# Kernel tuning notes

Measured on AMD Instinct MI355X. Metric: run time of the kernel, lower is better.

## Reference

```python
import jax, jax.numpy as jnp
import numpy as np

D_HEAD = 64
D_MODEL = 1024
N_HEADS = D_MODEL // D_HEAD
MAX_TOKENS = 2048


def setup_inputs() -> dict:
    key = jax.random.key(0)
    ks = jax.random.split(key, 5)
    batch, pos = 2, 2048
    # kaiming_normal_ on (n_heads, d_model, d_head): fan_in = d_model*d_head -> std = sqrt(2/fan_in)
    std_qkv = np.sqrt(2.0 / (D_MODEL * D_HEAD)).astype(np.float32)
    # xavier_normal_ on (d_model, d_model): std = sqrt(2/(fan_in+fan_out))
    std_out = np.sqrt(2.0 / (D_MODEL + D_MODEL)).astype(np.float32)
    return {
        "residual_stream": jax.random.normal(ks[0], (batch, pos, D_MODEL), dtype=jnp.float32),
        "weight_query": jax.random.normal(ks[1], (N_HEADS, D_MODEL, D_HEAD), dtype=jnp.float32) * std_qkv,
        "weight_key": jax.random.normal(ks[2], (N_HEADS, D_MODEL, D_HEAD), dtype=jnp.float32) * std_qkv,
        "weight_value": jax.random.normal(ks[3], (N_HEADS, D_MODEL, D_HEAD), dtype=jnp.float32) * std_qkv,
        "weight_out": jax.random.normal(ks[4], (D_MODEL, D_MODEL), dtype=jnp.float32) * std_out,
    }


def reference(residual_stream, weight_query, weight_key, weight_value, weight_out):
    # QKV projections: [b, p, m] x [h, m, d] -> [b, h, p, d]
    q = jnp.einsum('bpm,hmd->bhpd', residual_stream, weight_query)
    k = jnp.einsum('bpm,hmd->bhpd', residual_stream, weight_key)
    v = jnp.einsum('bpm,hmd->bhpd', residual_stream, weight_value)

    n_tokens = residual_stream.shape[1]
    # scaled scores [b, h, dest, src]
    scores = jnp.einsum('bhqd,bhkd->bhqk', q, k) / jnp.sqrt(jnp.float32(D_HEAD))
    # causal mask: -inf above the diagonal
    causal = jnp.tril(jnp.ones((n_tokens, n_tokens), dtype=bool))
    scores = jnp.where(causal, scores, jnp.float32(-jnp.inf))
    pattern = jax.nn.softmax(scores, axis=-1)

    attn = jnp.einsum('bhqk,bhkd->bhqd', pattern, v)  # [b, h, dest, d_head]
    # concat heads -> [b, p, h*d_head]
    b, h, p, d = attn.shape
    attn_concat = jnp.transpose(attn, (0, 2, 1, 3)).reshape(b, p, h * d)
    return jnp.einsum('bpm,mn->bpn', attn_concat, weight_out)
```

## Files before the change

kernel.cpp:

```cpp
#include <hip/hip_runtime.h>
#include <hip/hip_bf16.h>
#include <stdint.h>


typedef __bf16 bf16x8 __attribute__((ext_vector_type(8)));
typedef float f32x4 __attribute__((ext_vector_type(4)));
typedef unsigned short u16;

__device__ __forceinline__ u16 f2bf(float f) {
  unsigned u = __float_as_uint(f);
  u += 0x7fffu + ((u >> 16) & 1u);
  return (u16)(u >> 16);
}

__global__ __launch_bounds__(256) void xcvt_k(const float* __restrict__ in,
                                              u16* __restrict__ out) {
  int i = (blockIdx.x * 256 + threadIdx.x) * 8;
  float4 f0 = *reinterpret_cast<const float4*>(in + i);
  float4 f1 = *reinterpret_cast<const float4*>(in + i + 4);
  u16 tmp[8] = {f2bf(f0.x), f2bf(f0.y), f2bf(f0.z), f2bf(f0.w),
                f2bf(f1.x), f2bf(f1.y), f2bf(f1.z), f2bf(f1.w)};
  *reinterpret_cast<uint4*>(out + i) = *reinterpret_cast<uint4*>(tmp);
}

__global__ __launch_bounds__(256) void transpose_cvt_k(const float* __restrict__ in,
                                                       u16* __restrict__ out,
                                                       int R, int C) {
  __shared__ u16 tile[64][80];
  int b = blockIdx.z;
  int r0 = blockIdx.x * 64, c0 = blockIdx.y * 64;
  const float* ip = in + (size_t)b * R * C;
  u16* op = out + (size_t)b * R * C;
  int t = threadIdx.x;
  int r = t >> 2, cb = (t & 3) * 16;
  const float4* src = reinterpret_cast<const float4*>(ip + (size_t)(r0 + r) * C + c0 + cb);
  u16 tmp[16];
#pragma unroll
  for (int v = 0; v < 4; v++) {
    float4 f = src[v];
    tmp[v * 4 + 0] = f2bf(f.x);
    tmp[v * 4 + 1] = f2bf(f.y);
    tmp[v * 4 + 2] = f2bf(f.z);
    tmp[v * 4 + 3] = f2bf(f.w);
  }
  *reinterpret_cast<uint4*>(&tile[r][cb]) = *reinterpret_cast<uint4*>(&tmp[0]);
  *reinterpret_cast<uint4*>(&tile[r][cb + 8]) = *reinterpret_cast<uint4*>(&tmp[8]);
  __syncthreads();
  int c = t >> 2, rb = (t & 3) * 16;
  uint4 outv[2];
  u16* tp = reinterpret_cast<u16*>(outv);
#pragma unroll
  for (int j = 0; j < 16; j++) tp[j] = tile[rb + j][c];
  uint4* dst = reinterpret_cast<uint4*>(op + (size_t)(c0 + c) * R + r0 + rb);
  dst[0] = outv[0];
  dst[1] = outv[1];
}

__global__ __launch_bounds__(256) void transpose_qkv_k(const float* __restrict__ Wq,
                                                       const float* __restrict__ Wk,
                                                       const float* __restrict__ Wv,
                                                       u16* __restrict__ outBase) {
  __shared__ u16 tile[64][80];
  int z = blockIdx.z;
  int sel = z >> 4, head = z & 15;
  const float* W = (sel == 0) ? Wq : (sel == 1 ? Wk : Wv);
  const float* ip = W + (size_t)head * 65536;
  u16* op = outBase + (size_t)sel * 1048576 + (size_t)head * 65536;
  int r0 = blockIdx.x * 64;
  int t = threadIdx.x;
  int r = t >> 2, cb = (t & 3) * 16;
  const float4* src = reinterpret_cast<const float4*>(ip + (size_t)(r0 + r) * 64 + cb);
  u16 tmp[16];
#pragma unroll
  for (int v = 0; v < 4; v++) {
    float4 f = src[v];
    tmp[v * 4 + 0] = f2bf(f.x);
    tmp[v * 4 + 1] = f2bf(f.y);
    tmp[v * 4 + 2] = f2bf(f.z);
    tmp[v * 4 + 3] = f2bf(f.w);
  }
  *reinterpret_cast<uint4*>(&tile[r][cb]) = *reinterpret_cast<uint4*>(&tmp[0]);
  *reinterpret_cast<uint4*>(&tile[r][cb + 8]) = *reinterpret_cast<uint4*>(&tmp[8]);
  __syncthreads();
  int c = t >> 2, rb = (t & 3) * 16;
  uint4 outv[2];
  u16* tp = reinterpret_cast<u16*>(outv);
#pragma unroll
  for (int j = 0; j < 16; j++) tp[j] = tile[rb + j][c];
  uint4* dst = reinterpret_cast<uint4*>(op + (size_t)c * 1024 + r0 + rb);
  dst[0] = outv[0];
  dst[1] = outv[1];
}

__device__ __forceinline__ void gemm128_core(const u16* __restrict__ A,
                                             const u16* __restrict__ BT,
                                             int m0, int n0,
                                             f32x4 (&acc)[4][4]) {
  __shared__ u16 As[128][72];
  __shared__ u16 Bs[128][72];
  int t = threadIdx.x, l = t & 63;
  int w = t >> 6, wm = w & 1, wn = w >> 1;
  int l15 = l & 15, q4 = l >> 4;
  int sr = t >> 1, sch = (t & 1) * 32;
  f32x4 z4 = {0.f, 0.f, 0.f, 0.f};
#pragma unroll
  for (int mi = 0; mi < 4; mi++)
#pragma unroll
    for (int nt = 0; nt < 4; nt++) acc[mi][nt] = z4;

  for (int k0 = 0; k0 < 1024; k0 += 64) {
    __syncthreads();
    {
      const uint4* sa = reinterpret_cast<const uint4*>(A + (size_t)(m0 + sr) * 1024 + k0 + sch);
      const uint4* sb = reinterpret_cast<const uint4*>(BT + (size_t)(n0 + sr) * 1024 + k0 + sch);
      uint4 a0 = sa[0], a1 = sa[1], a2 = sa[2], a3 = sa[3];
      uint4 b0 = sb[0], b1 = sb[1], b2 = sb[2], b3 = sb[3];
      uint4* da = reinterpret_cast<uint4*>(&As[sr][sch]);
      da[0] = a0; da[1] = a1; da[2] = a2; da[3] = a3;
      uint4* db = reinterpret_cast<uint4*>(&Bs[sr][sch]);
      db[0] = b0; db[1] = b1; db[2] = b2; db[3] = b3;
    }
    __syncthreads();
#pragma unroll
    for (int kk = 0; kk < 2; kk++) {
      bf16x8 af[4], bfr[4];
#pragma unroll
      for (int mi = 0; mi < 4; mi++)
        af[mi] = *reinterpret_cast<const bf16x8*>(&As[wm * 64 + mi * 16 + l15][kk * 32 + q4 * 8]);
#pragma unroll
      for (int nt = 0; nt < 4; nt++)
        bfr[nt] = *reinterpret_cast<const bf16x8*>(&Bs[wn * 64 + nt * 16 + l15][kk * 32 + q4 * 8]);
#pragma unroll
      for (int mi = 0; mi < 4; mi++)
#pragma unroll
        for (int nt = 0; nt < 4; nt++)
          acc[mi][nt] = __builtin_amdgcn_mfma_f32_16x16x32_bf16(af[mi], bfr[nt], acc[mi][nt], 0, 0, 0);
    }
  }
}

__global__ __launch_bounds__(256) void qkv_gemm128_k(const u16* __restrict__ A,
                                                     const u16* __restrict__ BT,
                                                     u16* __restrict__ Q,
                                                     u16* __restrict__ K,
                                                     u16* __restrict__ VT2) {
  const float QSCALE = 0.125f * 1.44269504088896340736f;
  int m0 = blockIdx.x * 128, n0 = blockIdx.y * 128;
  f32x4 acc[4][4];
  gemm128_core(A, BT, m0, n0, acc);
  int t = threadIdx.x, l = t & 63;
  int w = t >> 6, wm = w & 1, wn = w >> 1;
  int l15 = l & 15, q4 = l >> 4;
#pragma unroll
  for (int mi = 0; mi < 4; mi++) {
#pragma unroll
    for (int nt = 0; nt < 4; nt++) {
#pragma unroll
      for (int r = 0; r < 4; r++) {
        int m = m0 + wm * 64 + mi * 16 + q4 * 4 + r;
        int n = n0 + wn * 64 + nt * 16 + l15;
        int wsel = n >> 10, h = (n >> 6) & 15, d = n & 63;
        int b = m >> 11, p = m & 2047;
        size_t bh = (size_t)(b * 16 + h);
        float v = acc[mi][nt][r];
        if (wsel == 0)
          Q[(bh * 2048 + p) * 64 + d] = f2bf(v * QSCALE);
        else if (wsel == 1)
          K[(bh * 2048 + p) * 64 + d] = f2bf(v);
        else
          VT2[((bh * 32 + (p >> 6)) * 64 + d) * 64 + (p & 63)] = f2bf(v);
      }
    }
  }
}

__global__ __launch_bounds__(256) void out_gemm128_k(const u16* __restrict__ A,
                                                     const u16* __restrict__ BT,
                                                     float* __restrict__ O) {
  int m0 = blockIdx.x * 128, n0 = blockIdx.y * 128;
  f32x4 acc[4][4];
  gemm128_core(A, BT, m0, n0, acc);
  int t = threadIdx.x, l = t & 63;
  int w = t >> 6, wm = w & 1, wn = w >> 1;
  int l15 = l & 15, q4 = l >> 4;
#pragma unroll
  for (int mi = 0; mi < 4; mi++) {
#pragma unroll
    for (int nt = 0; nt < 4; nt++) {
#pragma unroll
      for (int r = 0; r < 4; r++) {
        int m = m0 + wm * 64 + mi * 16 + q4 * 4 + r;
        int n = n0 + wn * 64 + nt * 16 + l15;
        O[(size_t)m * 1024 + n] = acc[mi][nt][r];
      }
    }
  }
}

__global__ __launch_bounds__(256) void attn_k(const u16* __restrict__ Q,
                                              const u16* __restrict__ K,
                                              const u16* __restrict__ VT2,
                                              u16* __restrict__ A) {
  __shared__ u16 Ks[2][64][72];
  __shared__ u16 Vs[2][64][72];
  __shared__ u16 P[4][16][72];
  int pr = blockIdx.x, h = blockIdx.y, b = blockIdx.z;
  size_t bh = (size_t)(b * 16 + h);
  const u16* Qp = Q + bh * 2048 * 64;
  const u16* Kp = K + bh * 2048 * 64;
  const u16* Vt = VT2 + bh * 32 * 64 * 64;
  int t = threadIdx.x, l = t & 63, w = t >> 6;
  int l15 = l & 15, q4 = l >> 4;
  const float NEG = -1e30f;
  f32x4 z4 = {0.f, 0.f, 0.f, 0.f};
  int srow = (t & 127) >> 1, shalf = t & 1;
  bool isV = t >= 128;
  const u16* sbase = (isV ? Vt : Kp) + (size_t)srow * 64 + shalf * 32;

#pragma unroll
  for (int which = 0; which < 2; which++) {
    int qt = which ? (31 - pr) : pr;
    int qrow = qt * 64 + w * 16 + l15;
    bf16x8 qf0 = *reinterpret_cast<const bf16x8*>(Qp + (size_t)qrow * 64 + q4 * 8);
    bf16x8 qf1 = *reinterpret_cast<const bf16x8*>(Qp + (size_t)qrow * 64 + 32 + q4 * 8);

    f32x4 accO[4] = {z4, z4, z4, z4};
    float rs[4] = {0.f, 0.f, 0.f, 0.f};

    {
      const uint4* s4 = reinterpret_cast<const uint4*>(sbase);
      uint4 v0 = s4[0], v1 = s4[1], v2 = s4[2], v3 = s4[3];
      uint4* d4 = isV ? reinterpret_cast<uint4*>(&Vs[0][srow][shalf * 32])
                      : reinterpret_cast<uint4*>(&Ks[0][srow][shalf * 32]);
      d4[0] = v0; d4[1] = v1; d4[2] = v2; d4[3] = v3;
    }
    __syncthreads();

    for (int kt = 0; kt <= qt; kt++) {
      int cur = kt & 1;
      bool more = kt < qt;
      uint4 n0, n1, n2, n3;
      if (more) {
        const uint4* s4 = reinterpret_cast<const uint4*>(sbase + (size_t)(kt + 1) * 4096);
        n0 = s4[0]; n1 = s4[1]; n2 = s4[2]; n3 = s4[3];
      }

      f32x4 s[4] = {z4, z4, z4, z4};
      __builtin_amdgcn_s_setprio(1);
#pragma unroll
      for (int kk = 0; kk < 2; kk++) {
        bf16x8 qa = (kk == 0) ? qf0 : qf1;
#pragma unroll
        for (int nt = 0; nt < 4; nt++) {
          bf16x8 kf = *reinterpret_cast<const bf16x8*>(&Ks[cur][nt * 16 + l15][kk * 32 + q4 * 8]);
          s[nt] = __builtin_amdgcn_mfma_f32_16x16x32_bf16(qa, kf, s[nt], 0, 0, 0);
        }
      }
      __builtin_amdgcn_s_setprio(0);
      if (kt == qt) {
        int rowl = w * 16 + q4 * 4;
#pragma unroll
        for (int nt = 0; nt < 4; nt++)
#pragma unroll
          for (int r = 0; r < 4; r++)
            if (nt * 16 + l15 > rowl + r) s[nt][r] = NEG;
      }
#pragma unroll
      for (int nt = 0; nt < 4; nt++)
#pragma unroll
        for (int r = 0; r < 4; r++) {
          float p = exp2f(s[nt][r]);
          rs[r] += p;
          P[w][q4 * 4 + r][nt * 16 + l15] = f2bf(p);
        }
      __builtin_amdgcn_s_setprio(1);
#pragma unroll
      for (int kk = 0; kk < 2; kk++) {
        bf16x8 pa = *reinterpret_cast<const bf16x8*>(&P[w][l15][kk * 32 + q4 * 8]);
#pragma unroll
        for (int nt = 0; nt < 4; nt++) {
          bf16x8 vf = *reinterpret_cast<const bf16x8*>(&Vs[cur][nt * 16 + l15][kk * 32 + q4 * 8]);
          accO[nt] = __builtin_amdgcn_mfma_f32_16x16x32_bf16(pa, vf, accO[nt], 0, 0, 0);
        }
      }
      __builtin_amdgcn_s_setprio(0);

      if (more) {
        uint4* d4 = isV ? reinterpret_cast<uint4*>(&Vs[cur ^ 1][srow][shalf * 32])
                        : reinterpret_cast<uint4*>(&Ks[cur ^ 1][srow][shalf * 32]);
        d4[0] = n0; d4[1] = n1; d4[2] = n2; d4[3] = n3;
      }
      __syncthreads();
    }
#pragma unroll
    for (int r = 0; r < 4; r++) {
#pragma unroll
      for (int sh = 1; sh < 16; sh <<= 1) rs[r] += __shfl_xor(rs[r], sh, 64);
      float inv = 1.f / rs[r];
      int prow = qt * 64 + w * 16 + q4 * 4 + r;
      size_t base = ((size_t)(b * 2048 + prow)) * 1024 + h * 64;
#pragma unroll
      for (int nt = 0; nt < 4; nt++) A[base + nt * 16 + l15] = f2bf(accO[nt][r] * inv);
    }
  }
}

extern "C" void kernel_launch(void* const* d_in, const int* in_sizes, int n_in,
                              void* d_out, int out_size, void* d_ws, size_t ws_size,
                              hipStream_t stream) {
  const float* X  = (const float*)d_in[0];
  const float* Wq = (const float*)d_in[1];
  const float* Wk = (const float*)d_in[2];
  const float* Wv = (const float*)d_in[3];
  const float* Wo = (const float*)d_in[4];
  float* out = (float*)d_out;

  u16* ws = (u16*)d_ws;
  u16* WqT = ws;
  u16* WoT = WqT + 3145728;
  u16* Xb  = WoT + 1048576;
  u16* Qb  = Xb + 4194304;
  u16* Kb  = Qb + 4194304;
  u16* VT2 = Kb + 4194304;
  u16* Ab  = Xb;

  xcvt_k<<<dim3(2048), 256, 0, stream>>>(X, Xb);
  transpose_qkv_k<<<dim3(16, 1, 48), 256, 0, stream>>>(Wq, Wk, Wv, WqT);
  transpose_cvt_k<<<dim3(16, 16, 1), 256, 0, stream>>>(Wo, WoT, 1024, 1024);

  qkv_gemm128_k<<<dim3(32, 24), 256, 0, stream>>>(Xb, WqT, Qb, Kb, VT2);
  attn_k<<<dim3(16, 16, 2), 256, 0, stream>>>(Qb, Kb, VT2, Ab);
  out_gemm128_k<<<dim3(32, 8), 256, 0, stream>>>(Ab, WoT, out);
}
```

Before: 205.3 us.

## Enlarge attention query tile to 128 rows and use direct global-to-LDS loads in GEMM

The attention kernel now handles 128 query rows per block, 32 per wave as two MFMA row groups. Each K/V tile in LDS is therefore reused across twice as many queries, and the grid is halved. Separately, the GEMM core stages A and B tiles with global_load_lds builtins into unpadded LDS arrays instead of loading through registers. The trade-offs are fewer blocks for occupancy and load balance in attention, more registers per wave, and possible LDS bank conflicts from the unpadded 64-wide rows.

```diff
diff --git a/kernel.cpp b/kernel.cpp
--- a/kernel.cpp
+++ b/kernel.cpp
@@ -92,16 +92,25 @@
   dst[1] = outv[1];
 }
 
+__device__ __forceinline__ void gload16(const u16* g, u16* l) {
+  __builtin_amdgcn_global_load_lds(
+      (__attribute__((address_space(1))) void*)(g),
+      (__attribute__((address_space(3))) void*)(l), 16, 0, 0);
+}
+
 __device__ __forceinline__ void gemm128_core(const u16* __restrict__ A,
                                              const u16* __restrict__ BT,
                                              int m0, int n0,
                                              f32x4 (&acc)[4][4]) {
-  __shared__ u16 As[128][72];
-  __shared__ u16 Bs[128][72];
+  __shared__ __align__(16) u16 As[128][64];
+  __shared__ __align__(16) u16 Bs[128][64];
   int t = threadIdx.x, l = t & 63;
   int w = t >> 6, wm = w & 1, wn = w >> 1;
   int l15 = l & 15, q4 = l >> 4;
-  int sr = t >> 1, sch = (t & 1) * 32;
+  int srow = w * 32 + (l >> 3);
+  int scol = (l & 7) * 8;
+  const u16* ga = A + (size_t)(m0 + srow) * 1024 + scol;
+  const u16* gb = BT + (size_t)(n0 + srow) * 1024 + scol;
   f32x4 z4 = {0.f, 0.f, 0.f, 0.f};
 #pragma unroll
   for (int mi = 0; mi < 4; mi++)
@@ -110,15 +119,10 @@
 
   for (int k0 = 0; k0 < 1024; k0 += 64) {
     __syncthreads();
-    {
-      const uint4* sa = reinterpret_cast<const uint4*>(A + (size_t)(m0 + sr) * 1024 + k0 + sch);
-      const uint4* sb = reinterpret_cast<const uint4*>(BT + (size_t)(n0 + sr) * 1024 + k0 + sch);
-      uint4 a0 = sa[0], a1 = sa[1], a2 = sa[2], a3 = sa[3];
-      uint4 b0 = sb[0], b1 = sb[1], b2 = sb[2], b3 = sb[3];
-      uint4* da = reinterpret_cast<uint4*>(&As[sr][sch]);
-      da[0] = a0; da[1] = a1; da[2] = a2; da[3] = a3;
-      uint4* db = reinterpret_cast<uint4*>(&Bs[sr][sch]);
-      db[0] = b0; db[1] = b1; db[2] = b2; db[3] = b3;
+#pragma unroll
+    for (int i = 0; i < 4; i++) {
+      gload16(ga + (size_t)(i * 8) * 1024 + k0, &As[w * 32 + i * 8][0]);
+      gload16(gb + (size_t)(i * 8) * 1024 + k0, &Bs[w * 32 + i * 8][0]);
     }
     __syncthreads();
 #pragma unroll
@@ -203,7 +207,7 @@
                                               u16* __restrict__ A) {
   __shared__ u16 Ks[2][64][72];
   __shared__ u16 Vs[2][64][72];
-  __shared__ u16 P[4][16][72];
+  __shared__ u16 P[4][32][80];
   int pr = blockIdx.x, h = blockIdx.y, b = blockIdx.z;
   size_t bh = (size_t)(b * 16 + h);
   const u16* Qp = Q + bh * 2048 * 64;
@@ -219,13 +223,25 @@
 
 #pragma unroll
   for (int which = 0; which < 2; which++) {
-    int qt = which ? (31 - pr) : pr;
-    int qrow = qt * 64 + w * 16 + l15;
-    bf16x8 qf0 = *reinterpret_cast<const bf16x8*>(Qp + (size_t)qrow * 64 + q4 * 8);
-    bf16x8 qf1 = *reinterpret_cast<const bf16x8*>(Qp + (size_t)qrow * 64 + 32 + q4 * 8);
-
-    f32x4 accO[4] = {z4, z4, z4, z4};
-    float rs[4] = {0.f, 0.f, 0.f, 0.f};
+    int qt = which ? (15 - pr) : pr;
+    int nkt = 2 * qt + 2;
+    int qr0 = qt * 128 + w * 32;
+    bf16x8 qf[2][2];
+#pragma unroll
+    for (int mi = 0; mi < 2; mi++) {
+      const u16* qp = Qp + (size_t)(qr0 + mi * 16 + l15) * 64;
+      qf[mi][0] = *reinterpret_cast<const bf16x8*>(qp + q4 * 8);
+      qf[mi][1] = *reinterpret_cast<const bf16x8*>(qp + 32 + q4 * 8);
+    }
+    f32x4 accO[2][4];
+    float rs[2][4];
+#pragma unroll
+    for (int mi = 0; mi < 2; mi++) {
+#pragma unroll
+      for (int nt = 0; nt < 4; nt++) accO[mi][nt] = z4;
+#pragma unroll
+      for (int r = 0; r < 4; r++) rs[mi][r] = 0.f;
+    }
 
     {
       const uint4* s4 = reinterpret_cast<const uint4*>(sbase);
@@ -236,51 +252,68 @@
     }
     __syncthreads();
 
-    for (int kt = 0; kt <= qt; kt++) {
+    for (int kt = 0; kt < nkt; kt++) {
       int cur = kt & 1;
-      bool more = kt < qt;
+      bool more = kt < nkt - 1;
       uint4 n0, n1, n2, n3;
       if (more) {
         const uint4* s4 = reinterpret_cast<const uint4*>(sbase + (size_t)(kt + 1) * 4096);
         n0 = s4[0]; n1 = s4[1]; n2 = s4[2]; n3 = s4[3];
       }
 
-      f32x4 s[4] = {z4, z4, z4, z4};
+      f32x4 s[2][4];
+#pragma unroll
+      for (int mi = 0; mi < 2; mi++)
+#pragma unroll
+        for (int nt = 0; nt < 4; nt++) s[mi][nt] = z4;
       __builtin_amdgcn_s_setprio(1);
 #pragma unroll
       for (int kk = 0; kk < 2; kk++) {
-        bf16x8 qa = (kk == 0) ? qf0 : qf1;
-#pragma unroll
-        for (int nt = 0; nt < 4; nt++) {
-          bf16x8 kf = *reinterpret_cast<const bf16x8*>(&Ks[cur][nt * 16 + l15][kk * 32 + q4 * 8]);
-          s[nt] = __builtin_amdgcn_mfma_f32_16x16x32_bf16(qa, kf, s[nt], 0, 0, 0);
-        }
+        bf16x8 kf[4];
+#pragma unroll
+        for (int nt = 0; nt < 4; nt++)
+          kf[nt] = *reinterpret_cast<const bf16x8*>(&Ks[cur][nt * 16 + l15][kk * 32 + q4 * 8]);
+#pragma unroll
+        for (int mi = 0; mi < 2; mi++)
+#pragma unroll
+          for (int nt = 0; nt < 4; nt++)
+            s[mi][nt] = __builtin_amdgcn_mfma_f32_16x16x32_bf16(qf[mi][kk], kf[nt], s[mi][nt], 0, 0, 0);
       }
       __builtin_amdgcn_s_setprio(0);
-      if (kt == qt) {
-        int rowl = w * 16 + q4 * 4;
+      if (kt >= 2 * qt) {
+        int colbase = (kt - 2 * qt) * 64;
+        int rowl = w * 32 + q4 * 4;
+#pragma unroll
+        for (int mi = 0; mi < 2; mi++)
+#pragma unroll
+          for (int nt = 0; nt < 4; nt++)
+#pragma unroll
+            for (int r = 0; r < 4; r++)
+              if (colbase + nt * 16 + l15 > rowl + mi * 16 + r) s[mi][nt][r] = NEG;
+      }
+#pragma unroll
+      for (int mi = 0; mi < 2; mi++)
 #pragma unroll
         for (int nt = 0; nt < 4; nt++)
 #pragma unroll
-          for (int r = 0; r < 4; r++)
-            if (nt * 16 + l15 > rowl + r) s[nt][r] = NEG;
-      }
-#pragma unroll
-      for (int nt = 0; nt < 4; nt++)
-#pragma unroll
-        for (int r = 0; r < 4; r++) {
-          float p = exp2f(s[nt][r]);
-          rs[r] += p;
-          P[w][q4 * 4 + r][nt * 16 + l15] = f2bf(p);
-        }
+          for (int r = 0; r < 4; r++) {
+            float p = exp2f(s[mi][nt][r]);
+            rs[mi][r] += p;
+            P[w][mi * 16 + q4 * 4 + r][nt * 16 + l15] = f2bf(p);
+          }
       __builtin_amdgcn_s_setprio(1);
 #pragma unroll
       for (int kk = 0; kk < 2; kk++) {
-        bf16x8 pa = *reinterpret_cast<const bf16x8*>(&P[w][l15][kk * 32 + q4 * 8]);
+        bf16x8 pa[2];
+#pragma unroll
+        for (int mi = 0; mi < 2; mi++)
+          pa[mi] = *reinterpret_cast<const bf16x8*>(&P[w][mi * 16 + l15][kk * 32 + q4 * 8]);
 #pragma unroll
         for (int nt = 0; nt < 4; nt++) {
           bf16x8 vf = *reinterpret_cast<const bf16x8*>(&Vs[cur][nt * 16 + l15][kk * 32 + q4 * 8]);
-          accO[nt] = __builtin_amdgcn_mfma_f32_16x16x32_bf16(pa, vf, accO[nt], 0, 0, 0);
+#pragma unroll
+          for (int mi = 0; mi < 2; mi++)
+            accO[mi][nt] = __builtin_amdgcn_mfma_f32_16x16x32_bf16(pa[mi], vf, accO[mi][nt], 0, 0, 0);
         }
       }
       __builtin_amdgcn_s_setprio(0);
@@ -293,15 +326,18 @@
       __syncthreads();
     }
 #pragma unroll
-    for (int r = 0; r < 4; r++) {
-#pragma unroll
-      for (int sh = 1; sh < 16; sh <<= 1) rs[r] += __shfl_xor(rs[r], sh, 64);
-      float inv = 1.f / rs[r];
-      int prow = qt * 64 + w * 16 + q4 * 4 + r;
-      size_t base = ((size_t)(b * 2048 + prow)) * 1024 + h * 64;
-#pragma unroll
-      for (int nt = 0; nt < 4; nt++) A[base + nt * 16 + l15] = f2bf(accO[nt][r] * inv);
-    }
+    for (int mi = 0; mi < 2; mi++)
+#pragma unroll
+      for (int r = 0; r < 4; r++) {
+        float v = rs[mi][r];
+#pragma unroll
+        for (int sh = 1; sh < 16; sh <<= 1) v += __shfl_xor(v, sh, 64);
+        float inv = 1.f / v;
+        int prow = qt * 128 + w * 32 + mi * 16 + q4 * 4 + r;
+        size_t base = ((size_t)(b * 2048 + prow)) * 1024 + h * 64;
+#pragma unroll
+        for (int nt = 0; nt < 4; nt++) A[base + nt * 16 + l15] = f2bf(accO[mi][nt][r] * inv);
+      }
   }
 }
 
@@ -329,6 +365,6 @@
   transpose_cvt_k<<<dim3(16, 16, 1), 256, 0, stream>>>(Wo, WoT, 1024, 1024);
 
   qkv_gemm128_k<<<dim3(32, 24), 256, 0, stream>>>(Xb, WqT, Qb, Kb, VT2);
-  attn_k<<<dim3(16, 16, 2), 256, 0, stream>>>(Qb, Kb, VT2, Ab);
+  attn_k<<<dim3(8, 16, 2), 256, 0, stream>>>(Qb, Kb, VT2, Ab);
   out_gemm128_k<<<dim3(32, 8), 256, 0, stream>>>(Ab, WoT, out);
 }
```

After: 227.0 us. 1.11x slower.
